# Kernel optimization log

Measured on AMD Instinct MI355X. Metric: run time of the kernel, lower is better.

## Reference

```python
import jax, jax.numpy as jnp
import numpy as np

N_QUBITS = 4
N_LAYERS = 2


def _apply_rx(state, theta, wire):
    """Apply RX(theta) on `wire`. state: [B] + [2]*n complex. theta: [B] or scalar."""
    n = state.ndim - 1
    ax = wire + 1
    half = jnp.asarray(theta) * 0.5
    c = jnp.cos(half)
    s = jnp.sin(half)
    # broadcast angle over the remaining qubit axes after taking the wire slice
    c = jnp.reshape(c, c.shape + (1,) * (n - 1))
    s = jnp.reshape(s, s.shape + (1,) * (n - 1))
    s0 = jnp.take(state, 0, axis=ax)
    s1 = jnp.take(state, 1, axis=ax)
    new0 = c * s0 - 1j * s * s1
    new1 = -1j * s * s0 + c * s1
    return jnp.stack([new0, new1], axis=ax)


def _apply_cnot(state, control, target):
    cax = control + 1
    tax = target + 1
    sub0 = jnp.take(state, 0, axis=cax)
    sub1 = jnp.take(state, 1, axis=cax)
    tax_sub = tax if tax < cax else tax - 1
    sub1 = jnp.flip(sub1, axis=tax_sub)  # X on target when control == 1
    return jnp.stack([sub0, sub1], axis=cax)


def _quantum_circuit(x, w):
    """AngleEmbedding(RX) + BasicEntanglerLayers(RX + CNOT ring), PauliZ expvals.
    x: [B, n_qubits] float32 angles; w: [n_layers, n_qubits] float32.
    Returns [B, n_qubits] float32."""
    B = x.shape[0]
    n = N_QUBITS
    state = jnp.zeros((B,) + (2,) * n, dtype=jnp.complex64)
    state = state.at[(slice(None),) + (0,) * n].set(1.0)
    # AngleEmbedding: RX(x_q) on wire q (per-sample angles)
    for q in range(n):
        state = _apply_rx(state, x[:, q], q)
    # BasicEntanglerLayers: per layer, RX(w[l,q]) on each wire then CNOT ring
    for l in range(N_LAYERS):
        for q in range(n):
            state = _apply_rx(state, w[l, q], q)
        for q in range(n):
            state = _apply_cnot(state, q, (q + 1) % n)
    probs = jnp.abs(state) ** 2  # [B, 2,2,2,2]
    flat = probs.reshape(B, -1)  # [B, 16]
    # <Z_q> = sum_b p(b) * (+1 if bit q == 0 else -1)
    bits = ((jnp.arange(2 ** n)[:, None] >> (n - 1 - jnp.arange(n))[None, :]) & 1)
    signs = (1.0 - 2.0 * bits).astype(jnp.float32)  # [16, n]
    return flat @ signs  # [B, n]


def setup_inputs() -> dict:
    key = jax.random.key(0)
    ks = jax.random.split(key, 5)
    B = 65536
    inputs = jax.random.normal(ks[0], (B, 28, 28), dtype=jnp.float32)
    W1 = jax.random.normal(ks[1], (784, N_QUBITS), dtype=jnp.float32) * 0.05
    b1 = jnp.zeros((N_QUBITS,), dtype=jnp.float32)
    qw = jax.random.normal(ks[2], (N_LAYERS, N_QUBITS), dtype=jnp.float32) * 0.1
    W2 = jax.random.normal(ks[3], (N_QUBITS, 32), dtype=jnp.float32) * 0.3
    b2 = jnp.zeros((32,), dtype=jnp.float32)
    W3 = jax.random.normal(ks[4], (32, 2), dtype=jnp.float32) * 0.2
    b3 = jnp.zeros((2,), dtype=jnp.float32)
    return {"inputs": inputs, "W1": W1, "b1": b1, "qw": qw, "W2": W2, "b2": b2, "W3": W3, "b3": b3}


def reference(inputs, W1, b1, qw, W2, b2, W3, b3):
    B = inputs.shape[0]
    flat = inputs.reshape(B, -1)                      # flatten
    pre = jax.nn.relu(flat @ W1 + b1)                 # dense_preprocess [B, 4]
    q = _quantum_circuit(pre, qw)                     # [B, 4]
    q = jnp.where(jnp.isnan(q), jnp.zeros_like(q), q)
    post = jax.nn.relu(q @ W2 + b2)                   # dense_postprocess [B, 32]
    return jax.nn.softmax(post @ W3 + b3, axis=-1)    # output_layer [B, 2]
```

## Files before the change

### kernel.cpp

```cpp
#include <hip/hip_runtime.h>
#include <math.h>


constexpr int ROW   = 784;
constexpr int ROW4  = 196;

__global__ __launch_bounds__(256) void gemv_pre_regw_kernel(
    const float* __restrict__ X,
    const float* __restrict__ W1,
    const float* __restrict__ b1,
    float* __restrict__ pre,
    int B)
{
    const int lane   = threadIdx.x & 63;
    const int waveG  = (blockIdx.x * 256 + threadIdx.x) >> 6;
    const int nWaves = (gridDim.x * 256) >> 6;
    const int nPair  = B >> 1;
    const bool tail  = (lane < 4);
    const int  jt    = 192 + (lane & 3);

    const float4* W1f4 = reinterpret_cast<const float4*>(W1);
    float4 w[4][4];
    #pragma unroll
    for (int i = 0; i < 4; i++) {
        const int j4 = (i < 3) ? (lane + (i << 6)) : jt;
        #pragma unroll
        for (int p = 0; p < 4; p++) w[i][p] = W1f4[4 * j4 + p];
    }
    const float bi0 = b1[0], bi1 = b1[1], bi2 = b1[2], bi3 = b1[3];

    const float4 zero4 = make_float4(0.f, 0.f, 0.f, 0.f);

    for (int t = waveG; t < nPair; t += nWaves) {
        const int s0 = t * 2;
        const float4* x0p = reinterpret_cast<const float4*>(X) + (size_t)s0 * ROW4;
        const float4* x1p = x0p + ROW4;

        float4 x0[4], x1[4];
        x0[0] = x0p[lane];       x1[0] = x1p[lane];
        x0[1] = x0p[lane + 64];  x1[1] = x1p[lane + 64];
        x0[2] = x0p[lane + 128]; x1[2] = x1p[lane + 128];
        x0[3] = tail ? x0p[192 + lane] : zero4;
        x1[3] = tail ? x1p[192 + lane] : zero4;

        float a0 = 0.f, a1 = 0.f, a2 = 0.f, a3 = 0.f;
        float c0 = 0.f, c1 = 0.f, c2 = 0.f, c3 = 0.f;
        #pragma unroll
        for (int i = 0; i < 4; i++) {
            a0 = fmaf(x0[i].x, w[i][0].x, a0); a1 = fmaf(x0[i].x, w[i][0].y, a1);
            a2 = fmaf(x0[i].x, w[i][0].z, a2); a3 = fmaf(x0[i].x, w[i][0].w, a3);
            c0 = fmaf(x1[i].x, w[i][0].x, c0); c1 = fmaf(x1[i].x, w[i][0].y, c1);
            c2 = fmaf(x1[i].x, w[i][0].z, c2); c3 = fmaf(x1[i].x, w[i][0].w, c3);
            a0 = fmaf(x0[i].y, w[i][1].x, a0); a1 = fmaf(x0[i].y, w[i][1].y, a1);
            a2 = fmaf(x0[i].y, w[i][1].z, a2); a3 = fmaf(x0[i].y, w[i][1].w, a3);
            c0 = fmaf(x1[i].y, w[i][1].x, c0); c1 = fmaf(x1[i].y, w[i][1].y, c1);
            c2 = fmaf(x1[i].y, w[i][1].z, c2); c3 = fmaf(x1[i].y, w[i][1].w, c3);
            a0 = fmaf(x0[i].z, w[i][2].x, a0); a1 = fmaf(x0[i].z, w[i][2].y, a1);
            a2 = fmaf(x0[i].z, w[i][2].z, a2); a3 = fmaf(x0[i].z, w[i][2].w, a3);
            c0 = fmaf(x1[i].z, w[i][2].x, c0); c1 = fmaf(x1[i].z, w[i][2].y, c1);
            c2 = fmaf(x1[i].z, w[i][2].z, c2); c3 = fmaf(x1[i].z, w[i][2].w, c3);
            a0 = fmaf(x0[i].w, w[i][3].x, a0); a1 = fmaf(x0[i].w, w[i][3].y, a1);
            a2 = fmaf(x0[i].w, w[i][3].z, a2); a3 = fmaf(x0[i].w, w[i][3].w, a3);
            c0 = fmaf(x1[i].w, w[i][3].x, c0); c1 = fmaf(x1[i].w, w[i][3].y, c1);
            c2 = fmaf(x1[i].w, w[i][3].z, c2); c3 = fmaf(x1[i].w, w[i][3].w, c3);
        }

        #pragma unroll
        for (int off = 32; off > 0; off >>= 1) {
            a0 += __shfl_xor(a0, off); c0 += __shfl_xor(c0, off);
            a1 += __shfl_xor(a1, off); c1 += __shfl_xor(c1, off);
            a2 += __shfl_xor(a2, off); c2 += __shfl_xor(c2, off);
            a3 += __shfl_xor(a3, off); c3 += __shfl_xor(c3, off);
        }
        if (lane == 0) {
            float4 r0, r1;
            r0.x = fmaxf(a0 + bi0, 0.f); r0.y = fmaxf(a1 + bi1, 0.f);
            r0.z = fmaxf(a2 + bi2, 0.f); r0.w = fmaxf(a3 + bi3, 0.f);
            r1.x = fmaxf(c0 + bi0, 0.f); r1.y = fmaxf(c1 + bi1, 0.f);
            r1.z = fmaxf(c2 + bi2, 0.f); r1.w = fmaxf(c3 + bi3, 0.f);
            float4* pp = reinterpret_cast<float4*>(pre) + s0;
            pp[0] = r0;
            pp[1] = r1;
        }
    }
}


__device__ __forceinline__ void apply_rx(float (&sr)[16], float (&si)[16],
                                         int mask, float c, float s)
{
    #pragma unroll
    for (int i = 0; i < 16; i++) {
        if (!(i & mask)) {
            int j = i | mask;
            float x0 = sr[i], y0 = si[i], x1 = sr[j], y1 = si[j];
            sr[i] = fmaf(c, x0,  s * y1);
            si[i] = fmaf(c, y0, -s * x1);
            sr[j] = fmaf(c, x1,  s * y0);
            si[j] = fmaf(c, y1, -s * x0);
        }
    }
}

__device__ __forceinline__ void apply_cnot(float (&sr)[16], float (&si)[16],
                                           int cmask, int tmask)
{
    #pragma unroll
    for (int i = 0; i < 16; i++) {
        if ((i & cmask) && !(i & tmask)) {
            int j = i | tmask;
            float tr = sr[i]; sr[i] = sr[j]; sr[j] = tr;
            float ti = si[i]; si[i] = si[j]; si[j] = ti;
        }
    }
}

__global__ __launch_bounds__(256) void epilogue_kernel(
    const float* __restrict__ pre,
    const float* __restrict__ qw,
    const float* __restrict__ W2,
    const float* __restrict__ b2,
    const float* __restrict__ W3,
    const float* __restrict__ b3,
    float* __restrict__ out,
    int B)
{
    int s = blockIdx.x * blockDim.x + threadIdx.x;
    if (s >= B) return;

    float4 ang = reinterpret_cast<const float4*>(pre)[s];

    float sr[16], si[16];
    #pragma unroll
    for (int i = 0; i < 16; i++) { sr[i] = 0.f; si[i] = 0.f; }
    sr[0] = 1.f;

    {
        float c, sn;
        __sincosf(ang.x * 0.5f, &sn, &c); apply_rx(sr, si, 8, c, sn);
        __sincosf(ang.y * 0.5f, &sn, &c); apply_rx(sr, si, 4, c, sn);
        __sincosf(ang.z * 0.5f, &sn, &c); apply_rx(sr, si, 2, c, sn);
        __sincosf(ang.w * 0.5f, &sn, &c); apply_rx(sr, si, 1, c, sn);
    }

    #pragma unroll
    for (int l = 0; l < 2; l++) {
        #pragma unroll
        for (int q = 0; q < 4; q++) {
            float c, sn;
            __sincosf(qw[l * 4 + q] * 0.5f, &sn, &c);
            apply_rx(sr, si, 8 >> q, c, sn);
        }
        apply_cnot(sr, si, 8, 4);
        apply_cnot(sr, si, 4, 2);
        apply_cnot(sr, si, 2, 1);
        apply_cnot(sr, si, 1, 8);
    }

    float z0 = 0.f, z1 = 0.f, z2 = 0.f, z3 = 0.f;
    #pragma unroll
    for (int i = 0; i < 16; i++) {
        float p = fmaf(sr[i], sr[i], si[i] * si[i]);
        z0 += (i & 8) ? -p : p;
        z1 += (i & 4) ? -p : p;
        z2 += (i & 2) ? -p : p;
        z3 += (i & 1) ? -p : p;
    }
    z0 = (z0 == z0) ? z0 : 0.f;
    z1 = (z1 == z1) ? z1 : 0.f;
    z2 = (z2 == z2) ? z2 : 0.f;
    z3 = (z3 == z3) ? z3 : 0.f;

    float l0 = b3[0], l1 = b3[1];
    #pragma unroll
    for (int k = 0; k < 32; k++) {
        float v = b2[k];
        v = fmaf(z0, W2[k],      v);
        v = fmaf(z1, W2[32 + k], v);
        v = fmaf(z2, W2[64 + k], v);
        v = fmaf(z3, W2[96 + k], v);
        v = fmaxf(v, 0.f);
        l0 = fmaf(v, W3[2 * k],     l0);
        l1 = fmaf(v, W3[2 * k + 1], l1);
    }

    float m  = fmaxf(l0, l1);
    float e0 = __expf(l0 - m), e1 = __expf(l1 - m);
    float inv = 1.f / (e0 + e1);
    reinterpret_cast<float2*>(out)[s] = make_float2(e0 * inv, e1 * inv);
}

extern "C" void kernel_launch(void* const* d_in, const int* in_sizes, int n_in,
                              void* d_out, int out_size, void* d_ws, size_t ws_size,
                              hipStream_t stream)
{
    const float* X  = (const float*)d_in[0];
    const float* W1 = (const float*)d_in[1];
    const float* b1 = (const float*)d_in[2];
    const float* qw = (const float*)d_in[3];
    const float* W2 = (const float*)d_in[4];
    const float* b2 = (const float*)d_in[5];
    const float* W3 = (const float*)d_in[6];
    const float* b3 = (const float*)d_in[7];

    const int B = in_sizes[0] / ROW;
    float* pre = (float*)d_ws;

    gemv_pre_regw_kernel<<<2048, 256, 0, stream>>>(X, W1, b1, pre, B);
    epilogue_kernel<<<(B + 255) / 256, 256, 0, stream>>>(pre, qw, W2, b2, W3, b3,
                                                         (float*)d_out, B);
}
```

Before: 294.0 us.

## Fuse GEMV and quantum epilogue into one kernel with butterfly reduction

Merges the preprocessing GEMV and the quantum-circuit/MLP epilogue into a single kernel, which drops the second launch and the round trip of the intermediate activations through global memory. Each wave now handles 8 samples per iteration, double-buffering the row loads, and reduces the 32 partial sums with a transpose-style butterfly of shuffles instead of separate full reductions. The epilogue then runs on only 8 lanes per wave, which idles most lanes during the circuit math, and the larger register footprint may lower occupancy for this bandwidth-bound read of X.

```diff
diff --git a/kernel.cpp b/kernel.cpp
--- a/kernel.cpp
+++ b/kernel.cpp
@@ -2,89 +2,8 @@
 #include <math.h>
 
 
-constexpr int ROW   = 784;
-constexpr int ROW4  = 196;
-
-__global__ __launch_bounds__(256) void gemv_pre_regw_kernel(
-    const float* __restrict__ X,
-    const float* __restrict__ W1,
-    const float* __restrict__ b1,
-    float* __restrict__ pre,
-    int B)
-{
-    const int lane   = threadIdx.x & 63;
-    const int waveG  = (blockIdx.x * 256 + threadIdx.x) >> 6;
-    const int nWaves = (gridDim.x * 256) >> 6;
-    const int nPair  = B >> 1;
-    const bool tail  = (lane < 4);
-    const int  jt    = 192 + (lane & 3);
-
-    const float4* W1f4 = reinterpret_cast<const float4*>(W1);
-    float4 w[4][4];
-    #pragma unroll
-    for (int i = 0; i < 4; i++) {
-        const int j4 = (i < 3) ? (lane + (i << 6)) : jt;
-        #pragma unroll
-        for (int p = 0; p < 4; p++) w[i][p] = W1f4[4 * j4 + p];
-    }
-    const float bi0 = b1[0], bi1 = b1[1], bi2 = b1[2], bi3 = b1[3];
-
-    const float4 zero4 = make_float4(0.f, 0.f, 0.f, 0.f);
-
-    for (int t = waveG; t < nPair; t += nWaves) {
-        const int s0 = t * 2;
-        const float4* x0p = reinterpret_cast<const float4*>(X) + (size_t)s0 * ROW4;
-        const float4* x1p = x0p + ROW4;
-
-        float4 x0[4], x1[4];
-        x0[0] = x0p[lane];       x1[0] = x1p[lane];
-        x0[1] = x0p[lane + 64];  x1[1] = x1p[lane + 64];
-        x0[2] = x0p[lane + 128]; x1[2] = x1p[lane + 128];
-        x0[3] = tail ? x0p[192 + lane] : zero4;
-        x1[3] = tail ? x1p[192 + lane] : zero4;
-
-        float a0 = 0.f, a1 = 0.f, a2 = 0.f, a3 = 0.f;
-        float c0 = 0.f, c1 = 0.f, c2 = 0.f, c3 = 0.f;
-        #pragma unroll
-        for (int i = 0; i < 4; i++) {
-            a0 = fmaf(x0[i].x, w[i][0].x, a0); a1 = fmaf(x0[i].x, w[i][0].y, a1);
-            a2 = fmaf(x0[i].x, w[i][0].z, a2); a3 = fmaf(x0[i].x, w[i][0].w, a3);
-            c0 = fmaf(x1[i].x, w[i][0].x, c0); c1 = fmaf(x1[i].x, w[i][0].y, c1);
-            c2 = fmaf(x1[i].x, w[i][0].z, c2); c3 = fmaf(x1[i].x, w[i][0].w, c3);
-            a0 = fmaf(x0[i].y, w[i][1].x, a0); a1 = fmaf(x0[i].y, w[i][1].y, a1);
-            a2 = fmaf(x0[i].y, w[i][1].z, a2); a3 = fmaf(x0[i].y, w[i][1].w, a3);
-            c0 = fmaf(x1[i].y, w[i][1].x, c0); c1 = fmaf(x1[i].y, w[i][1].y, c1);
-            c2 = fmaf(x1[i].y, w[i][1].z, c2); c3 = fmaf(x1[i].y, w[i][1].w, c3);
-            a0 = fmaf(x0[i].z, w[i][2].x, a0); a1 = fmaf(x0[i].z, w[i][2].y, a1);
-            a2 = fmaf(x0[i].z, w[i][2].z, a2); a3 = fmaf(x0[i].z, w[i][2].w, a3);
-            c0 = fmaf(x1[i].z, w[i][2].x, c0); c1 = fmaf(x1[i].z, w[i][2].y, c1);
-            c2 = fmaf(x1[i].z, w[i][2].z, c2); c3 = fmaf(x1[i].z, w[i][2].w, c3);
-            a0 = fmaf(x0[i].w, w[i][3].x, a0); a1 = fmaf(x0[i].w, w[i][3].y, a1);
-            a2 = fmaf(x0[i].w, w[i][3].z, a2); a3 = fmaf(x0[i].w, w[i][3].w, a3);
-            c0 = fmaf(x1[i].w, w[i][3].x, c0); c1 = fmaf(x1[i].w, w[i][3].y, c1);
-            c2 = fmaf(x1[i].w, w[i][3].z, c2); c3 = fmaf(x1[i].w, w[i][3].w, c3);
-        }
-
-        #pragma unroll
-        for (int off = 32; off > 0; off >>= 1) {
-            a0 += __shfl_xor(a0, off); c0 += __shfl_xor(c0, off);
-            a1 += __shfl_xor(a1, off); c1 += __shfl_xor(c1, off);
-            a2 += __shfl_xor(a2, off); c2 += __shfl_xor(c2, off);
-            a3 += __shfl_xor(a3, off); c3 += __shfl_xor(c3, off);
-        }
-        if (lane == 0) {
-            float4 r0, r1;
-            r0.x = fmaxf(a0 + bi0, 0.f); r0.y = fmaxf(a1 + bi1, 0.f);
-            r0.z = fmaxf(a2 + bi2, 0.f); r0.w = fmaxf(a3 + bi3, 0.f);
-            r1.x = fmaxf(c0 + bi0, 0.f); r1.y = fmaxf(c1 + bi1, 0.f);
-            r1.z = fmaxf(c2 + bi2, 0.f); r1.w = fmaxf(c3 + bi3, 0.f);
-            float4* pp = reinterpret_cast<float4*>(pre) + s0;
-            pp[0] = r0;
-            pp[1] = r1;
-        }
-    }
-}
-
+constexpr int ROW  = 784;
+constexpr int ROW4 = 196;
 
 __device__ __forceinline__ void apply_rx(float (&sr)[16], float (&si)[16],
                                          int mask, float c, float s)
@@ -115,8 +34,34 @@
     }
 }
 
-__global__ __launch_bounds__(256) void epilogue_kernel(
-    const float* __restrict__ pre,
+#define FMA_ONE(xv, wrow, o0) \
+    a[(o0)+0] = fmaf(xv, wrow.x, a[(o0)+0]); \
+    a[(o0)+1] = fmaf(xv, wrow.y, a[(o0)+1]); \
+    a[(o0)+2] = fmaf(xv, wrow.z, a[(o0)+2]); \
+    a[(o0)+3] = fmaf(xv, wrow.w, a[(o0)+3]);
+
+#define FMA_ROUND(xb, o0, o1) { \
+    _Pragma("unroll") \
+    for (int i = 0; i < 4; i++) { \
+        FMA_ONE(xb[i].x,     w[i][0], o0) FMA_ONE(xb[4+i].x, w[i][0], o1) \
+        FMA_ONE(xb[i].y,     w[i][1], o0) FMA_ONE(xb[4+i].y, w[i][1], o1) \
+        FMA_ONE(xb[i].z,     w[i][2], o0) FMA_ONE(xb[4+i].z, w[i][2], o1) \
+        FMA_ONE(xb[i].w,     w[i][3], o0) FMA_ONE(xb[4+i].w, w[i][3], o1) \
+    } }
+
+#define LOAD_ROUND(dst, sA, sB) { \
+    const float4* p0_ = X4 + (size_t)(sA) * ROW4; \
+    const float4* p1_ = X4 + (size_t)(sB) * ROW4; \
+    dst[0] = p0_[lane];        dst[4] = p1_[lane]; \
+    dst[1] = p0_[lane + 64];   dst[5] = p1_[lane + 64]; \
+    dst[2] = p0_[lane + 128];  dst[6] = p1_[lane + 128]; \
+    dst[3] = tail ? p0_[192 + lane] : zero4; \
+    dst[7] = tail ? p1_[192 + lane] : zero4; }
+
+__global__ __launch_bounds__(256) void fused_kernel(
+    const float* __restrict__ X,
+    const float* __restrict__ W1,
+    const float* __restrict__ b1,
     const float* __restrict__ qw,
     const float* __restrict__ W2,
     const float* __restrict__ b2,
@@ -125,69 +70,164 @@
     float* __restrict__ out,
     int B)
 {
-    int s = blockIdx.x * blockDim.x + threadIdx.x;
-    if (s >= B) return;
-
-    float4 ang = reinterpret_cast<const float4*>(pre)[s];
-
-    float sr[16], si[16];
+    const int lane = threadIdx.x & 63;
+    const int wid  = (blockIdx.x * 256 + threadIdx.x) >> 6;
+    const int nW   = (gridDim.x * 256) >> 6;
+    const bool tail = (lane < 4);
+    const int  jt   = 192 + (lane & 3);
+
+    const float4* X4   = reinterpret_cast<const float4*>(X);
+    const float4* W1f4 = reinterpret_cast<const float4*>(W1);
+
+    float4 w[4][4];
     #pragma unroll
-    for (int i = 0; i < 16; i++) { sr[i] = 0.f; si[i] = 0.f; }
-    sr[0] = 1.f;
-
-    {
-        float c, sn;
-        __sincosf(ang.x * 0.5f, &sn, &c); apply_rx(sr, si, 8, c, sn);
-        __sincosf(ang.y * 0.5f, &sn, &c); apply_rx(sr, si, 4, c, sn);
-        __sincosf(ang.z * 0.5f, &sn, &c); apply_rx(sr, si, 2, c, sn);
-        __sincosf(ang.w * 0.5f, &sn, &c); apply_rx(sr, si, 1, c, sn);
-    }
-
-    #pragma unroll
-    for (int l = 0; l < 2; l++) {
-        #pragma unroll
-        for (int q = 0; q < 4; q++) {
-            float c, sn;
-            __sincosf(qw[l * 4 + q] * 0.5f, &sn, &c);
-            apply_rx(sr, si, 8 >> q, c, sn);
-        }
-        apply_cnot(sr, si, 8, 4);
-        apply_cnot(sr, si, 4, 2);
-        apply_cnot(sr, si, 2, 1);
-        apply_cnot(sr, si, 1, 8);
-    }
-
-    float z0 = 0.f, z1 = 0.f, z2 = 0.f, z3 = 0.f;
-    #pragma unroll
-    for (int i = 0; i < 16; i++) {
-        float p = fmaf(sr[i], sr[i], si[i] * si[i]);
-        z0 += (i & 8) ? -p : p;
-        z1 += (i & 4) ? -p : p;
-        z2 += (i & 2) ? -p : p;
-        z3 += (i & 1) ? -p : p;
-    }
-    z0 = (z0 == z0) ? z0 : 0.f;
-    z1 = (z1 == z1) ? z1 : 0.f;
-    z2 = (z2 == z2) ? z2 : 0.f;
-    z3 = (z3 == z3) ? z3 : 0.f;
-
-    float l0 = b3[0], l1 = b3[1];
-    #pragma unroll
-    for (int k = 0; k < 32; k++) {
-        float v = b2[k];
-        v = fmaf(z0, W2[k],      v);
-        v = fmaf(z1, W2[32 + k], v);
-        v = fmaf(z2, W2[64 + k], v);
-        v = fmaf(z3, W2[96 + k], v);
-        v = fmaxf(v, 0.f);
-        l0 = fmaf(v, W3[2 * k],     l0);
-        l1 = fmaf(v, W3[2 * k + 1], l1);
-    }
-
-    float m  = fmaxf(l0, l1);
-    float e0 = __expf(l0 - m), e1 = __expf(l1 - m);
-    float inv = 1.f / (e0 + e1);
-    reinterpret_cast<float2*>(out)[s] = make_float2(e0 * inv, e1 * inv);
+    for (int i = 0; i < 4; i++) {
+        const int j4 = (i < 3) ? (lane + (i << 6)) : jt;
+        #pragma unroll
+        for (int p = 0; p < 4; p++) w[i][p] = W1f4[4 * j4 + p];
+    }
+
+    const int idx = ((lane >> 5) & 1) * 16 + ((lane >> 4) & 1) * 8 +
+                    ((lane >> 3) & 1) * 4  + ((lane >> 2) & 1) * 2 +
+                    ((lane >> 1) & 1);
+    const float bl = b1[idx & 3];
+
+    const bool b5  = (lane & 32) != 0;
+    const bool b4  = (lane & 16) != 0;
+    const bool b3f = (lane & 8)  != 0;
+    const bool b2f = (lane & 4)  != 0;
+    const bool b1f = (lane & 2)  != 0;
+
+    const float4 zero4 = make_float4(0.f, 0.f, 0.f, 0.f);
+    const int sl = B - 1;
+
+    for (int S = wid * 8; S < B; S += nW * 8) {
+        const int s0 = (S     < sl) ? S     : sl;
+        const int s1 = (S + 1 < sl) ? S + 1 : sl;
+        const int s2 = (S + 2 < sl) ? S + 2 : sl;
+        const int s3 = (S + 3 < sl) ? S + 3 : sl;
+        const int s4 = (S + 4 < sl) ? S + 4 : sl;
+        const int s5 = (S + 5 < sl) ? S + 5 : sl;
+        const int s6 = (S + 6 < sl) ? S + 6 : sl;
+        const int s7 = (S + 7 < sl) ? S + 7 : sl;
+
+        float a[32];
+        #pragma unroll
+        for (int i = 0; i < 32; i++) a[i] = 0.f;
+
+        float4 xA[8], xB[8];
+        LOAD_ROUND(xA, s0, s1)
+        LOAD_ROUND(xB, s2, s3)
+        FMA_ROUND(xA, 0, 4)
+        LOAD_ROUND(xA, s4, s5)
+        FMA_ROUND(xB, 8, 12)
+        LOAD_ROUND(xB, s6, s7)
+        FMA_ROUND(xA, 16, 20)
+        FMA_ROUND(xB, 24, 28)
+
+        float v16[16];
+        #pragma unroll
+        for (int i = 0; i < 16; i++) {
+            float kv = b5 ? a[i + 16] : a[i];
+            float sv = b5 ? a[i]      : a[i + 16];
+            v16[i] = kv + __shfl_xor(sv, 32);
+        }
+        float v8a[8];
+        #pragma unroll
+        for (int i = 0; i < 8; i++) {
+            float kv = b4 ? v16[i + 8] : v16[i];
+            float sv = b4 ? v16[i]     : v16[i + 8];
+            v8a[i] = kv + __shfl_xor(sv, 16);
+        }
+        float v4a[4];
+        #pragma unroll
+        for (int i = 0; i < 4; i++) {
+            float kv = b3f ? v8a[i + 4] : v8a[i];
+            float sv = b3f ? v8a[i]     : v8a[i + 4];
+            v4a[i] = kv + __shfl_xor(sv, 8);
+        }
+        float v2a[2];
+        #pragma unroll
+        for (int i = 0; i < 2; i++) {
+            float kv = b2f ? v4a[i + 2] : v4a[i];
+            float sv = b2f ? v4a[i]     : v4a[i + 2];
+            v2a[i] = kv + __shfl_xor(sv, 4);
+        }
+        float kv = b1f ? v2a[1] : v2a[0];
+        float sv = b1f ? v2a[0] : v2a[1];
+        float v1 = kv + __shfl_xor(sv, 2);
+        v1 += __shfl_xor(v1, 1);
+
+        const float pre_val = fmaxf(v1 + bl, 0.f);
+
+        const float p0 = __shfl(pre_val, ((lane & 7) << 3) + 0);
+        const float p1 = __shfl(pre_val, ((lane & 7) << 3) + 2);
+        const float p2 = __shfl(pre_val, ((lane & 7) << 3) + 4);
+        const float p3 = __shfl(pre_val, ((lane & 7) << 3) + 6);
+
+        if (lane < 8 && S + lane < B) {
+            const int s = S + lane;
+
+            float sr[16], si[16];
+            #pragma unroll
+            for (int i = 0; i < 16; i++) { sr[i] = 0.f; si[i] = 0.f; }
+            sr[0] = 1.f;
+
+            {
+                float c, sn;
+                __sincosf(p0 * 0.5f, &sn, &c); apply_rx(sr, si, 8, c, sn);
+                __sincosf(p1 * 0.5f, &sn, &c); apply_rx(sr, si, 4, c, sn);
+                __sincosf(p2 * 0.5f, &sn, &c); apply_rx(sr, si, 2, c, sn);
+                __sincosf(p3 * 0.5f, &sn, &c); apply_rx(sr, si, 1, c, sn);
+            }
+
+            #pragma unroll
+            for (int l = 0; l < 2; l++) {
+                #pragma unroll
+                for (int q = 0; q < 4; q++) {
+                    float c, sn;
+                    __sincosf(qw[l * 4 + q] * 0.5f, &sn, &c);
+                    apply_rx(sr, si, 8 >> q, c, sn);
+                }
+                apply_cnot(sr, si, 8, 4);
+                apply_cnot(sr, si, 4, 2);
+                apply_cnot(sr, si, 2, 1);
+                apply_cnot(sr, si, 1, 8);
+            }
+
+            float z0 = 0.f, z1 = 0.f, z2 = 0.f, z3 = 0.f;
+            #pragma unroll
+            for (int i = 0; i < 16; i++) {
+                float p = fmaf(sr[i], sr[i], si[i] * si[i]);
+                z0 += (i & 8) ? -p : p;
+                z1 += (i & 4) ? -p : p;
+                z2 += (i & 2) ? -p : p;
+                z3 += (i & 1) ? -p : p;
+            }
+            z0 = (z0 == z0) ? z0 : 0.f;
+            z1 = (z1 == z1) ? z1 : 0.f;
+            z2 = (z2 == z2) ? z2 : 0.f;
+            z3 = (z3 == z3) ? z3 : 0.f;
+
+            float l0 = b3[0], l1 = b3[1];
+            #pragma unroll
+            for (int k = 0; k < 32; k++) {
+                float v = b2[k];
+                v = fmaf(z0, W2[k],      v);
+                v = fmaf(z1, W2[32 + k], v);
+                v = fmaf(z2, W2[64 + k], v);
+                v = fmaf(z3, W2[96 + k], v);
+                v = fmaxf(v, 0.f);
+                l0 = fmaf(v, W3[2 * k],     l0);
+                l1 = fmaf(v, W3[2 * k + 1], l1);
+            }
+
+            float m  = fmaxf(l0, l1);
+            float e0 = __expf(l0 - m), e1 = __expf(l1 - m);
+            float inv = 1.f / (e0 + e1);
+            reinterpret_cast<float2*>(out)[s] = make_float2(e0 * inv, e1 * inv);
+        }
+    }
 }
 
 extern "C" void kernel_launch(void* const* d_in, const int* in_sizes, int n_in,
@@ -204,9 +244,7 @@
     const float* b3 = (const float*)d_in[7];
 
     const int B = in_sizes[0] / ROW;
-    float* pre = (float*)d_ws;
-
-    gemv_pre_regw_kernel<<<2048, 256, 0, stream>>>(X, W1, b1, pre, B);
-    epilogue_kernel<<<(B + 255) / 256, 256, 0, stream>>>(pre, qw, W2, b2, W3, b3,
-                                                         (float*)d_out, B);
-}
+
+    fused_kernel<<<2048, 256, 0, stream>>>(X, W1, b1, qw, W2, b2, W3, b3,
+                                           (float*)d_out, B);
+}
```

Result: no change. 293.0 us (-0.4%).

## Fuse input projection into quantum epilogue with one thread per sample

Applied to the files above, without the earlier changes.

Replaces the two-kernel pipeline with a single kernel. Each thread now computes its own 784-long dot product against W1, streaming its row through an 8-deep float4 register prefetch buffer, then runs the quantum simulation and MLP head. This removes the intermediate `pre` buffer round trip, the second launch and the wave-level shuffle reductions. In exchange, each thread strides across a separate 3 KB row, so loads within a wave are no longer coalesced. With only one thread per sample the grid has just 256 blocks, which leaves little parallelism to hide memory latency.

```diff
diff --git a/kernel.cpp b/kernel.cpp
--- a/kernel.cpp
+++ b/kernel.cpp
@@ -2,89 +2,8 @@
 #include <math.h>
 
 
-constexpr int ROW   = 784;
-constexpr int ROW4  = 196;
-
-__global__ __launch_bounds__(256) void gemv_pre_regw_kernel(
-    const float* __restrict__ X,
-    const float* __restrict__ W1,
-    const float* __restrict__ b1,
-    float* __restrict__ pre,
-    int B)
-{
-    const int lane   = threadIdx.x & 63;
-    const int waveG  = (blockIdx.x * 256 + threadIdx.x) >> 6;
-    const int nWaves = (gridDim.x * 256) >> 6;
-    const int nPair  = B >> 1;
-    const bool tail  = (lane < 4);
-    const int  jt    = 192 + (lane & 3);
-
-    const float4* W1f4 = reinterpret_cast<const float4*>(W1);
-    float4 w[4][4];
-    #pragma unroll
-    for (int i = 0; i < 4; i++) {
-        const int j4 = (i < 3) ? (lane + (i << 6)) : jt;
-        #pragma unroll
-        for (int p = 0; p < 4; p++) w[i][p] = W1f4[4 * j4 + p];
-    }
-    const float bi0 = b1[0], bi1 = b1[1], bi2 = b1[2], bi3 = b1[3];
-
-    const float4 zero4 = make_float4(0.f, 0.f, 0.f, 0.f);
-
-    for (int t = waveG; t < nPair; t += nWaves) {
-        const int s0 = t * 2;
-        const float4* x0p = reinterpret_cast<const float4*>(X) + (size_t)s0 * ROW4;
-        const float4* x1p = x0p + ROW4;
-
-        float4 x0[4], x1[4];
-        x0[0] = x0p[lane];       x1[0] = x1p[lane];
-        x0[1] = x0p[lane + 64];  x1[1] = x1p[lane + 64];
-        x0[2] = x0p[lane + 128]; x1[2] = x1p[lane + 128];
-        x0[3] = tail ? x0p[192 + lane] : zero4;
-        x1[3] = tail ? x1p[192 + lane] : zero4;
-
-        float a0 = 0.f, a1 = 0.f, a2 = 0.f, a3 = 0.f;
-        float c0 = 0.f, c1 = 0.f, c2 = 0.f, c3 = 0.f;
-        #pragma unroll
-        for (int i = 0; i < 4; i++) {
-            a0 = fmaf(x0[i].x, w[i][0].x, a0); a1 = fmaf(x0[i].x, w[i][0].y, a1);
-            a2 = fmaf(x0[i].x, w[i][0].z, a2); a3 = fmaf(x0[i].x, w[i][0].w, a3);
-            c0 = fmaf(x1[i].x, w[i][0].x, c0); c1 = fmaf(x1[i].x, w[i][0].y, c1);
-            c2 = fmaf(x1[i].x, w[i][0].z, c2); c3 = fmaf(x1[i].x, w[i][0].w, c3);
-            a0 = fmaf(x0[i].y, w[i][1].x, a0); a1 = fmaf(x0[i].y, w[i][1].y, a1);
-            a2 = fmaf(x0[i].y, w[i][1].z, a2); a3 = fmaf(x0[i].y, w[i][1].w, a3);
-            c0 = fmaf(x1[i].y, w[i][1].x, c0); c1 = fmaf(x1[i].y, w[i][1].y, c1);
-            c2 = fmaf(x1[i].y, w[i][1].z, c2); c3 = fmaf(x1[i].y, w[i][1].w, c3);
-            a0 = fmaf(x0[i].z, w[i][2].x, a0); a1 = fmaf(x0[i].z, w[i][2].y, a1);
-            a2 = fmaf(x0[i].z, w[i][2].z, a2); a3 = fmaf(x0[i].z, w[i][2].w, a3);
-            c0 = fmaf(x1[i].z, w[i][2].x, c0); c1 = fmaf(x1[i].z, w[i][2].y, c1);
-            c2 = fmaf(x1[i].z, w[i][2].z, c2); c3 = fmaf(x1[i].z, w[i][2].w, c3);
-            a0 = fmaf(x0[i].w, w[i][3].x, a0); a1 = fmaf(x0[i].w, w[i][3].y, a1);
-            a2 = fmaf(x0[i].w, w[i][3].z, a2); a3 = fmaf(x0[i].w, w[i][3].w, a3);
-            c0 = fmaf(x1[i].w, w[i][3].x, c0); c1 = fmaf(x1[i].w, w[i][3].y, c1);
-            c2 = fmaf(x1[i].w, w[i][3].z, c2); c3 = fmaf(x1[i].w, w[i][3].w, c3);
-        }
-
-        #pragma unroll
-        for (int off = 32; off > 0; off >>= 1) {
-            a0 += __shfl_xor(a0, off); c0 += __shfl_xor(c0, off);
-            a1 += __shfl_xor(a1, off); c1 += __shfl_xor(c1, off);
-            a2 += __shfl_xor(a2, off); c2 += __shfl_xor(c2, off);
-            a3 += __shfl_xor(a3, off); c3 += __shfl_xor(c3, off);
-        }
-        if (lane == 0) {
-            float4 r0, r1;
-            r0.x = fmaxf(a0 + bi0, 0.f); r0.y = fmaxf(a1 + bi1, 0.f);
-            r0.z = fmaxf(a2 + bi2, 0.f); r0.w = fmaxf(a3 + bi3, 0.f);
-            r1.x = fmaxf(c0 + bi0, 0.f); r1.y = fmaxf(c1 + bi1, 0.f);
-            r1.z = fmaxf(c2 + bi2, 0.f); r1.w = fmaxf(c3 + bi3, 0.f);
-            float4* pp = reinterpret_cast<float4*>(pre) + s0;
-            pp[0] = r0;
-            pp[1] = r1;
-        }
-    }
-}
-
+constexpr int ROW  = 784;
+constexpr int ROW4 = 196;
 
 __device__ __forceinline__ void apply_rx(float (&sr)[16], float (&si)[16],
                                          int mask, float c, float s)
@@ -115,8 +34,33 @@
     }
 }
 
-__global__ __launch_bounds__(256) void epilogue_kernel(
-    const float* __restrict__ pre,
+#define FMAS(x, wA, wB, wC, wD) \
+    a0 = fmaf(x.x, wA.x, a0); a1 = fmaf(x.x, wA.y, a1); \
+    a2 = fmaf(x.x, wA.z, a2); a3 = fmaf(x.x, wA.w, a3); \
+    a0 = fmaf(x.y, wB.x, a0); a1 = fmaf(x.y, wB.y, a1); \
+    a2 = fmaf(x.y, wB.z, a2); a3 = fmaf(x.y, wB.w, a3); \
+    a0 = fmaf(x.z, wC.x, a0); a1 = fmaf(x.z, wC.y, a1); \
+    a2 = fmaf(x.z, wC.z, a2); a3 = fmaf(x.z, wC.w, a3); \
+    a0 = fmaf(x.w, wD.x, a0); a1 = fmaf(x.w, wD.y, a1); \
+    a2 = fmaf(x.w, wD.z, a2); a3 = fmaf(x.w, wD.w, a3);
+
+#define STEP_R(slot, k) { \
+    const float4 x = xb[slot]; \
+    xb[slot] = xr[(k) + 8]; \
+    const float4 wA = Wf4[4*(k)+0], wB = Wf4[4*(k)+1], \
+                 wC = Wf4[4*(k)+2], wD = Wf4[4*(k)+3]; \
+    FMAS(x, wA, wB, wC, wD) }
+
+#define STEP_N(slot, k) { \
+    const float4 x = xb[slot]; \
+    const float4 wA = Wf4[4*(k)+0], wB = Wf4[4*(k)+1], \
+                 wC = Wf4[4*(k)+2], wD = Wf4[4*(k)+3]; \
+    FMAS(x, wA, wB, wC, wD) }
+
+__global__ __launch_bounds__(256) void fused_kernel(
+    const float* __restrict__ X,
+    const float* __restrict__ W1,
+    const float* __restrict__ b1,
     const float* __restrict__ qw,
     const float* __restrict__ W2,
     const float* __restrict__ b2,
@@ -125,10 +69,34 @@
     float* __restrict__ out,
     int B)
 {
-    int s = blockIdx.x * blockDim.x + threadIdx.x;
+    const int s = blockIdx.x * blockDim.x + threadIdx.x;
     if (s >= B) return;
 
-    float4 ang = reinterpret_cast<const float4*>(pre)[s];
+    const float4* __restrict__ xr  = reinterpret_cast<const float4*>(X)
+                                     + (size_t)s * ROW4;
+    const float4* __restrict__ Wf4 = reinterpret_cast<const float4*>(W1);
+
+    float a0 = 0.f, a1 = 0.f, a2 = 0.f, a3 = 0.f;
+
+    float4 xb[8];
+    #pragma unroll
+    for (int i = 0; i < 8; i++) xb[i] = xr[i];
+
+    int k = 0;
+    #pragma unroll 1
+    for (int m = 0; m < 23; m++) {
+        STEP_R(0, k + 0) STEP_R(1, k + 1) STEP_R(2, k + 2) STEP_R(3, k + 3)
+        STEP_R(4, k + 4) STEP_R(5, k + 5) STEP_R(6, k + 6) STEP_R(7, k + 7)
+        k += 8;
+    }
+    STEP_R(0, 184) STEP_R(1, 185) STEP_R(2, 186) STEP_R(3, 187)
+    STEP_N(4, 188) STEP_N(5, 189) STEP_N(6, 190) STEP_N(7, 191)
+    STEP_N(0, 192) STEP_N(1, 193) STEP_N(2, 194) STEP_N(3, 195)
+
+    const float p0 = fmaxf(a0 + b1[0], 0.f);
+    const float p1 = fmaxf(a1 + b1[1], 0.f);
+    const float p2 = fmaxf(a2 + b1[2], 0.f);
+    const float p3 = fmaxf(a3 + b1[3], 0.f);
 
     float sr[16], si[16];
     #pragma unroll
@@ -137,10 +105,10 @@
 
     {
         float c, sn;
-        __sincosf(ang.x * 0.5f, &sn, &c); apply_rx(sr, si, 8, c, sn);
-        __sincosf(ang.y * 0.5f, &sn, &c); apply_rx(sr, si, 4, c, sn);
-        __sincosf(ang.z * 0.5f, &sn, &c); apply_rx(sr, si, 2, c, sn);
-        __sincosf(ang.w * 0.5f, &sn, &c); apply_rx(sr, si, 1, c, sn);
+        __sincosf(p0 * 0.5f, &sn, &c); apply_rx(sr, si, 8, c, sn);
+        __sincosf(p1 * 0.5f, &sn, &c); apply_rx(sr, si, 4, c, sn);
+        __sincosf(p2 * 0.5f, &sn, &c); apply_rx(sr, si, 2, c, sn);
+        __sincosf(p3 * 0.5f, &sn, &c); apply_rx(sr, si, 1, c, sn);
     }
 
     #pragma unroll
@@ -173,15 +141,15 @@
 
     float l0 = b3[0], l1 = b3[1];
     #pragma unroll
-    for (int k = 0; k < 32; k++) {
-        float v = b2[k];
-        v = fmaf(z0, W2[k],      v);
-        v = fmaf(z1, W2[32 + k], v);
-        v = fmaf(z2, W2[64 + k], v);
-        v = fmaf(z3, W2[96 + k], v);
+    for (int kk = 0; kk < 32; kk++) {
+        float v = b2[kk];
+        v = fmaf(z0, W2[kk],      v);
+        v = fmaf(z1, W2[32 + kk], v);
+        v = fmaf(z2, W2[64 + kk], v);
+        v = fmaf(z3, W2[96 + kk], v);
         v = fmaxf(v, 0.f);
-        l0 = fmaf(v, W3[2 * k],     l0);
-        l1 = fmaf(v, W3[2 * k + 1], l1);
+        l0 = fmaf(v, W3[2 * kk],     l0);
+        l1 = fmaf(v, W3[2 * kk + 1], l1);
     }
 
     float m  = fmaxf(l0, l1);
@@ -204,9 +172,8 @@
     const float* b3 = (const float*)d_in[7];
 
     const int B = in_sizes[0] / ROW;
-    float* pre = (float*)d_ws;
 
-    gemv_pre_regw_kernel<<<2048, 256, 0, stream>>>(X, W1, b1, pre, B);
-    epilogue_kernel<<<(B + 255) / 256, 256, 0, stream>>>(pre, qw, W2, b2, W3, b3,
-                                                         (float*)d_out, B);
+    const int blocks = (B + 255) / 256;
+    fused_kernel<<<blocks, 256, 0, stream>>>(X, W1, b1, qw, W2, b2, W3, b3,
+                                             (float*)d_out, B);
 }
```

Measured after the change: 295.6 us. No clear change (+0.6%).
